# Kernel tuning notes

Measured on AMD Instinct MI355X. Metric: run time of the kernel, lower is better.

## Reference

```python
import jax, jax.numpy as jnp
import numpy as np

SEQ_LEN = 1024
INPUT_DIM = 1
HIDDEN_DIM = 512
OUTPUT_DIM = 10
BATCH = 512  # must equal HIDDEN_DIM (original code broadcasts h[H,H] + hx(x)[B,H])


def setup_inputs() -> dict:
    key = jax.random.key(0)
    ks = jax.random.split(key, 7)
    s_hx = 1.0 / np.sqrt(INPUT_DIM)
    s_hh = 1.0 / np.sqrt(HIDDEN_DIM)
    s_oh = 1.0 / np.sqrt(HIDDEN_DIM)
    return {
        "x": jax.random.normal(ks[0], (BATCH, SEQ_LEN), dtype=jnp.float32),
        "W_hx": jax.random.uniform(ks[1], (HIDDEN_DIM, INPUT_DIM), jnp.float32, -s_hx, s_hx),
        "b_hx": jax.random.uniform(ks[2], (HIDDEN_DIM,), jnp.float32, -s_hx, s_hx),
        "W_hh": jax.random.uniform(ks[3], (HIDDEN_DIM, HIDDEN_DIM), jnp.float32, -s_hh, s_hh),
        "b_hh": jax.random.uniform(ks[4], (HIDDEN_DIM,), jnp.float32, -s_hh, s_hh),
        "W_oh": jax.random.uniform(ks[5], (OUTPUT_DIM, HIDDEN_DIM), jnp.float32, -s_oh, s_oh),
        "b_oh": jax.random.uniform(ks[6], (OUTPUT_DIM,), jnp.float32, -s_oh, s_oh),
    }


def reference(x, W_hx, b_hx, W_hh, b_hh, W_oh, b_oh):
    # x: [B, S]; original unsqueezes to [B, S, 1] and loops t=0..S-1:
    #   h = tanh(hx(x[:, t]) + hh(h)),  h init zeros[H, H] (B == H)
    # Precompute the input projection for all timesteps (input_dim == 1):
    # hx(x[:, t]) = x[:, t, None] @ W_hx.T + b_hx -> [B, H]
    xs = x[:, :, None] * W_hx[None, None, :, 0] + b_hx  # [B, S, H]
    xs = jnp.swapaxes(xs, 0, 1)  # [S, B, H] for scan

    h0 = jnp.zeros((HIDDEN_DIM, HIDDEN_DIM), dtype=jnp.float32)

    def step(h, x_t):
        h = jnp.tanh(x_t + h @ W_hh.T + b_hh)
        return h, None

    h, _ = jax.lax.scan(step, h0, xs)
    o = h @ W_oh.T + b_oh  # [B, O]
    return jax.nn.softmax(o, axis=1)
```

## Files before the change

kernel.cpp:

```cpp
#include <hip/hip_runtime.h>

#define SEQ   1024
#define HID   512
#define OUTD  10
#define RPB   16
#define NRG   32
#define NCG   2
#define CPB   (HID/NCG)
#define NWV   8
#define CPWV  (CPB/NWV)
#define NT    (CPWV/16)
#define NKT   (HID/32)
#define OKT   (NKT/NCG)
#define PCP   (CPB/2)
#define PANEL (RPB*PCP)

typedef float f32x4  __attribute__((ext_vector_type(4)));
typedef short bf16x8 __attribute__((ext_vector_type(8)));
typedef int   i32x4  __attribute__((ext_vector_type(4)));
typedef unsigned long long u64;

__device__ __forceinline__ unsigned short f2bf(float f) {
    unsigned u = __builtin_bit_cast(unsigned, f);
    u += 0x7fffu + ((u >> 16) & 1u);
    return (unsigned short)(u >> 16);
}
__device__ __forceinline__ float bf2f(unsigned short s) {
    return __builtin_bit_cast(float, ((unsigned)s) << 16);
}

__device__ __forceinline__ size_t panel_base(int buf, int cg, int rg) {
    return (((size_t)buf * NCG + cg) * NRG + rg) * PANEL;
}

__global__ __launch_bounds__(512, 2) void rnn_kernel(
    const float* __restrict__ x,
    const float* __restrict__ W_hx,
    const float* __restrict__ b_hx,
    const float* __restrict__ W_hh,
    const float* __restrict__ b_hh,
    const float* __restrict__ W_oh,
    const float* __restrict__ b_oh,
    float* __restrict__ out,
    u64* __restrict__ hX)
{
    __shared__ unsigned short hL[RPB * HID];
    __shared__ float obuf[RPB][OUTD];
    char* const hLb = (char*)hL;

    const int tid  = threadIdx.x;
    const int lane = tid & 63;
    const int wv   = tid >> 6;
    const int bid  = blockIdx.x;
    const int rg   = bid & (NRG - 1);
    const int cg   = bid >> 5;
    const int row0 = rg * RPB;
    const int crow = lane & 15;
    const int kb   = lane >> 4;
    const int dr0  = kb * 4;
    const int amask = (crow & 7) << 4;

    int ktmap[NKT];
#pragma unroll
    for (int j = 0; j < OKT; ++j) {
        ktmap[j]       = cg * OKT + j;
        ktmap[OKT + j] = (cg ^ 1) * OKT + j;
    }

    bf16x8 wfr[NT][NKT];
    float  whx[NT], bc[NT];
#pragma unroll
    for (int nt = 0; nt < NT; ++nt) {
        const int col = cg * CPB + wv * CPWV + nt * 16 + crow;
        whx[nt] = W_hx[col];
        bc[nt]  = b_hx[col] + b_hh[col];
#pragma unroll
        for (int j = 0; j < NKT; ++j) {
            const float* p = W_hh + (size_t)col * HID + ktmap[j] * 32 + kb * 8;
            bf16x8 v;
#pragma unroll
            for (int e = 0; e < 8; ++e) v[e] = (short)f2bf(p[e]);
            wfr[nt][j] = v;
        }
    }

    const int prow  = tid >> 5;
    const int pcp0  = (tid & 31) * 4;
    auto poll_fill = [&](int buf, unsigned want) {
        const u64* rp = hX + panel_base(buf, cg ^ 1, rg) + tid * 4;
        u64 vals[4];
        for (;;) {
            u64 v = __hip_atomic_load(rp, __ATOMIC_RELAXED,
                                      __HIP_MEMORY_SCOPE_AGENT);
            if ((unsigned)(v >> 32) == want) { vals[0] = v; break; }
            __builtin_amdgcn_s_sleep(1);
        }
        unsigned need = 0xEu;
        while (need) {
#pragma unroll
            for (int j = 1; j < 4; ++j) {
                const unsigned b = 1u << j;
                if (need & b) {
                    u64 v = __hip_atomic_load(rp + j, __ATOMIC_RELAXED,
                                              __HIP_MEMORY_SCOPE_AGENT);
                    if ((unsigned)(v >> 32) == want) { vals[j] = v; need &= ~b; }
                }
            }
            if (need) __builtin_amdgcn_s_sleep(1);
        }
        i32x4 w;
#pragma unroll
        for (int j = 0; j < 4; ++j) w[j] = (int)(unsigned)vals[j];
        int ad = (prow * 1024 + (cg ^ 1) * 512 + pcp0 * 4) ^ ((prow & 7) << 4);
        *(i32x4*)(hLb + ad) = w;
    };

    f32x4 acc[NT];

    for (int t = 0; t < SEQ; ++t) {
        float xv[4];
#pragma unroll
        for (int r = 0; r < 4; ++r)
            xv[r] = x[(size_t)(row0 + dr0 + r) * SEQ + t];

#pragma unroll
        for (int nt = 0; nt < NT; ++nt) acc[nt] = (f32x4){0.f, 0.f, 0.f, 0.f};

        if (t > 0) {
#pragma unroll
            for (int j = 0; j < OKT; ++j) {
                int ad = (crow * 1024 + ktmap[j] * 64 + kb * 16) ^ amask;
                bf16x8 a = *(const bf16x8*)(hLb + ad);
                acc[0] = __builtin_amdgcn_mfma_f32_16x16x32_bf16(a, wfr[0][j], acc[0], 0, 0, 0);
                acc[1] = __builtin_amdgcn_mfma_f32_16x16x32_bf16(a, wfr[1][j], acc[1], 0, 0, 0);
            }
            poll_fill(t & 1, (unsigned)t);
            __syncthreads();
#pragma unroll
            for (int j = OKT; j < NKT; ++j) {
                int ad = (crow * 1024 + ktmap[j] * 64 + kb * 16) ^ amask;
                bf16x8 a = *(const bf16x8*)(hLb + ad);
                acc[0] = __builtin_amdgcn_mfma_f32_16x16x32_bf16(a, wfr[0][j], acc[0], 0, 0, 0);
                acc[1] = __builtin_amdgcn_mfma_f32_16x16x32_bf16(a, wfr[1][j], acc[1], 0, 0, 0);
            }
        }

        u64* const wp = hX + panel_base((t + 1) & 1, cg, rg);
        const u64 tag = ((u64)(unsigned)(t + 1)) << 32;
#pragma unroll
        for (int nt = 0; nt < NT; ++nt) {
#pragma unroll
            for (int r = 0; r < 4; ++r) {
                float pre = acc[nt][r] + xv[r] * whx[nt] + bc[nt];
                float e   = __expf(2.0f * pre);
                float h   = 1.0f - 2.0f / (e + 1.0f);
                unsigned hu = f2bf(h);
                unsigned pv = __shfl_xor(hu, 1);
                if (!(crow & 1)) {
                    unsigned payload = hu | (pv << 16);
                    const int row = dr0 + r;
                    const int cpl = wv * 16 + nt * 8 + (crow >> 1);
                    __hip_atomic_store(wp + row * PCP + cpl, payload | tag,
                                       __ATOMIC_RELAXED, __HIP_MEMORY_SCOPE_AGENT);
                    int ad = (row * 1024 + (cg * CPB + wv * CPWV + nt * 16 + crow) * 2)
                             ^ ((row & 7) << 4);
                    *(unsigned*)(hLb + ad) = payload;
                }
            }
        }
        __syncthreads();
    }

    if (cg != 0) return;
    poll_fill(SEQ & 1, (unsigned)SEQ);
    __syncthreads();

    if (tid < RPB * OUTD) {
        const int bl = tid / OUTD, j = tid % OUTD;
        const float* wrow = W_oh + (size_t)j * HID;
        float s = b_oh[j];
        for (int k = 0; k < HID; ++k) {
            int ad = (bl * 1024 + k * 2) ^ ((bl & 7) << 4);
            s += bf2f(*(const unsigned short*)(hLb + ad)) * wrow[k];
        }
        obuf[bl][j] = s;
    }
    __syncthreads();
    if (tid < RPB) {
        float m = -1e30f;
#pragma unroll
        for (int j = 0; j < OUTD; ++j) m = fmaxf(m, obuf[tid][j]);
        float e[OUTD], ss = 0.f;
#pragma unroll
        for (int j = 0; j < OUTD; ++j) { e[j] = __expf(obuf[tid][j] - m); ss += e[j]; }
        float inv = 1.0f / ss;
#pragma unroll
        for (int j = 0; j < OUTD; ++j)
            out[(size_t)(row0 + tid) * OUTD + j] = e[j] * inv;
    }
}

extern "C" void kernel_launch(void* const* d_in, const int* in_sizes, int n_in,
                              void* d_out, int out_size, void* d_ws, size_t ws_size,
                              hipStream_t stream) {
    (void)in_sizes; (void)n_in; (void)out_size; (void)ws_size;
    const float* x    = (const float*)d_in[0];
    const float* W_hx = (const float*)d_in[1];
    const float* b_hx = (const float*)d_in[2];
    const float* W_hh = (const float*)d_in[3];
    const float* b_hh = (const float*)d_in[4];
    const float* W_oh = (const float*)d_in[5];
    const float* b_oh = (const float*)d_in[6];
    float* out = (float*)d_out;
    u64* hX = (u64*)d_ws;

    rnn_kernel<<<dim3(NRG * NCG), dim3(512), 0, stream>>>(
        x, W_hx, b_hx, W_hh, b_hh, W_oh, b_oh, out, hX);
}
```

Measured before the change: 3.072 ms.

## Detect same-XCC sibling blocks and use plain volatile exchange for them

At start each block reads its XCC ID from a hardware register, publishes it to a workspace table, and checks whether its sibling column-group block runs on the same XCC. If so, the per-step hidden-state exchange uses volatile 64-bit stores and vectorized 128-bit volatile polling loads instead of agent-scope atomics, aiming to cut cross-block handoff latency. It relies on a shared XCC L2 giving coherence for volatile accesses, and the workspace table is never reset, so a stale 0x5A5A tag left from an earlier launch could yield a wrong same-XCC decision.

```diff
diff --git a/kernel.cpp b/kernel.cpp
--- a/kernel.cpp
+++ b/kernel.cpp
@@ -42,10 +42,12 @@
     const float* __restrict__ W_oh,
     const float* __restrict__ b_oh,
     float* __restrict__ out,
-    u64* __restrict__ hX)
+    u64* __restrict__ hX,
+    unsigned* __restrict__ xtab)
 {
     __shared__ unsigned short hL[RPB * HID];
     __shared__ float obuf[RPB][OUTD];
+    __shared__ int sameLDS;
     char* const hLb = (char*)hL;
 
     const int tid  = threadIdx.x;
@@ -60,6 +62,21 @@
     const int dr0  = kb * 4;
     const int amask = (crow & 7) << 4;
 
+    if (tid == 0) {
+        unsigned xcc;
+        asm volatile("s_getreg_b32 %0, hwreg(HW_REG_XCC_ID)" : "=s"(xcc));
+        xcc &= 0xFu;
+        __hip_atomic_store(&xtab[bid], 0x5A5A0000u | xcc, __ATOMIC_RELAXED,
+                           __HIP_MEMORY_SCOPE_AGENT);
+        const int sib = (cg ^ 1) * NRG + rg;
+        unsigned v;
+        do {
+            v = __hip_atomic_load(&xtab[sib], __ATOMIC_RELAXED,
+                                  __HIP_MEMORY_SCOPE_AGENT);
+        } while ((v & 0xFFFF0000u) != 0x5A5A0000u);
+        sameLDS = ((v & 0xFu) == xcc) ? 1 : 0;
+    }
+
     int ktmap[NKT];
 #pragma unroll
     for (int j = 0; j < OKT; ++j) {
@@ -84,33 +101,50 @@
         }
     }
 
-    const int prow  = tid >> 5;
-    const int pcp0  = (tid & 31) * 4;
+    __syncthreads();
+    const bool nearp = (sameLDS != 0);
+
+    const int prow = tid >> 5;
+    const int pcp0 = (tid & 31) * 4;
     auto poll_fill = [&](int buf, unsigned want) {
         const u64* rp = hX + panel_base(buf, cg ^ 1, rg) + tid * 4;
-        u64 vals[4];
-        for (;;) {
-            u64 v = __hip_atomic_load(rp, __ATOMIC_RELAXED,
-                                      __HIP_MEMORY_SCOPE_AGENT);
-            if ((unsigned)(v >> 32) == want) { vals[0] = v; break; }
-            __builtin_amdgcn_s_sleep(1);
-        }
-        unsigned need = 0xEu;
-        while (need) {
-#pragma unroll
-            for (int j = 1; j < 4; ++j) {
-                const unsigned b = 1u << j;
-                if (need & b) {
-                    u64 v = __hip_atomic_load(rp + j, __ATOMIC_RELAXED,
-                                              __HIP_MEMORY_SCOPE_AGENT);
-                    if ((unsigned)(v >> 32) == want) { vals[j] = v; need &= ~b; }
+        i32x4 w;
+        if (nearp) {
+            volatile const i32x4* vp = (volatile const i32x4*)rp;
+            for (;;) {
+                i32x4 a = vp[0];
+                i32x4 b = vp[1];
+                if ((unsigned)a[1] == want && (unsigned)a[3] == want &&
+                    (unsigned)b[1] == want && (unsigned)b[3] == want) {
+                    w[0] = a[0]; w[1] = a[2]; w[2] = b[0]; w[3] = b[2];
+                    break;
                 }
-            }
-            if (need) __builtin_amdgcn_s_sleep(1);
-        }
-        i32x4 w;
-#pragma unroll
-        for (int j = 0; j < 4; ++j) w[j] = (int)(unsigned)vals[j];
+                __builtin_amdgcn_s_sleep(1);
+            }
+        } else {
+            u64 vals[4];
+            for (;;) {
+                u64 v = __hip_atomic_load(rp, __ATOMIC_RELAXED,
+                                          __HIP_MEMORY_SCOPE_AGENT);
+                if ((unsigned)(v >> 32) == want) { vals[0] = v; break; }
+                __builtin_amdgcn_s_sleep(1);
+            }
+            unsigned need = 0xEu;
+            while (need) {
+#pragma unroll
+                for (int j = 1; j < 4; ++j) {
+                    const unsigned b = 1u << j;
+                    if (need & b) {
+                        u64 v = __hip_atomic_load(rp + j, __ATOMIC_RELAXED,
+                                                  __HIP_MEMORY_SCOPE_AGENT);
+                        if ((unsigned)(v >> 32) == want) { vals[j] = v; need &= ~b; }
+                    }
+                }
+                if (need) __builtin_amdgcn_s_sleep(1);
+            }
+#pragma unroll
+            for (int j = 0; j < 4; ++j) w[j] = (int)(unsigned)vals[j];
+        }
         int ad = (prow * 1024 + (cg ^ 1) * 512 + pcp0 * 4) ^ ((prow & 7) << 4);
         *(i32x4*)(hLb + ad) = w;
     };
@@ -160,8 +194,11 @@
                     unsigned payload = hu | (pv << 16);
                     const int row = dr0 + r;
                     const int cpl = wv * 16 + nt * 8 + (crow >> 1);
-                    __hip_atomic_store(wp + row * PCP + cpl, payload | tag,
-                                       __ATOMIC_RELAXED, __HIP_MEMORY_SCOPE_AGENT);
+                    u64* p = wp + row * PCP + cpl;
+                    u64 word = (u64)payload | tag;
+                    if (nearp) *(volatile u64*)p = word;
+                    else __hip_atomic_store(p, word, __ATOMIC_RELAXED,
+                                            __HIP_MEMORY_SCOPE_AGENT);
                     int ad = (row * 1024 + (cg * CPB + wv * CPWV + nt * 16 + crow) * 2)
                              ^ ((row & 7) << 4);
                     *(unsigned*)(hLb + ad) = payload;
@@ -213,7 +250,8 @@
     const float* b_oh = (const float*)d_in[6];
     float* out = (float*)d_out;
     u64* hX = (u64*)d_ws;
+    unsigned* xtab = (unsigned*)((char*)d_ws + 2u * 1024 * 1024);
 
     rnn_kernel<<<dim3(NRG * NCG), dim3(512), 0, stream>>>(
-        x, W_hx, b_hx, W_hh, b_hh, W_oh, b_oh, out, hX);
-}
+        x, W_hx, b_hx, W_hh, b_hh, W_oh, b_oh, out, hX, xtab);
+}
```

Result: slower. 5.007 ms (+63.0%).
